# Performance work log

Measured on AMD Instinct MI355X. Metric: run time of the kernel, lower is better.

## Reference

```python
import jax, jax.numpy as jnp
import numpy as np

B, L, H, NT = 16, 2048, 512, 8
HEAD_H = max(32, H // 2)
OUT = 2 * H + NT
LN_EPS = 1e-5


def setup_inputs() -> dict:
    key = jax.random.key(0)
    ks = jax.random.split(key, 32)
    def w(i, shape):
        fan_in = shape[0] if len(shape) > 1 else shape[0]
        return jax.random.normal(ks[i], shape, jnp.float32) / np.sqrt(fan_in)
    z = lambda shape: jnp.zeros(shape, jnp.float32)
    return {
        "x": jax.random.normal(ks[0], (B, L, 2), jnp.float32),
        "t": jax.random.uniform(ks[1], (B, L, 1), jnp.float32),
        "Wt1": w(2, (1, NT)), "bt1": z((NT,)),
        "Wt2": w(3, (NT, NT)), "bt2": z((NT,)),
        "Wpf": w(4, (2 + NT, H)), "bpf": z((H,)),
        "Wpb": w(5, (2 + NT, H)), "bpb": z((H,)),
        "Wzf": w(6, (H, H)), "bzf": z((H,)),
        "Whf": w(7, (H, H)), "bhf": z((H,)),
        "Wzb": w(8, (H, H)), "bzb": z((H,)),
        "Whb": w(9, (H, H)), "bhb": z((H,)),
        "ln_g": jnp.ones((OUT,), jnp.float32), "ln_b": z((OUT,)),
        "time_scale": jnp.array(5.0, jnp.float32),
        "Wg1": w(10, (OUT, HEAD_H)), "bg1": z((HEAD_H,)),
        "Wg2": w(11, (HEAD_H, 1)), "bg2": z((1,)),
    }


def _mingru_states(xc, Wp, bp, Wz, bz, Wh, bh):
    """Run minGRU over xc (B,L,D); return h_prev states: out[:,ti] = h before step ti."""
    inp = xc @ Wp + bp                      # (B,L,H)
    zg = jax.nn.sigmoid(inp @ Wz + bz)
    h_tilde = jnp.tanh(inp @ Wh + bh)
    a = 1.0 - zg                            # decay
    b = zg * h_tilde                        # input injection
    def step(h, ab):
        h = ab[0] * h + ab[1]
        return h, h
    h0 = jnp.zeros((xc.shape[0], Wh.shape[1]), xc.dtype)
    _, hs = jax.lax.scan(step, h0, (jnp.moveaxis(a, 1, 0), jnp.moveaxis(b, 1, 0)))
    hs = jnp.moveaxis(hs, 0, 1)             # (B,L,H), hs[:,ti] = h after step ti
    # Original stores h_prev at each position -> shift right with zero prefix.
    return jnp.concatenate([jnp.zeros_like(hs[:, :1]), hs[:, :-1]], axis=1)


def reference(x, t, Wt1, bt1, Wt2, bt2, Wpf, bpf, Wpb, bpb,
              Wzf, bzf, Whf, bhf, Wzb, bzb, Whb, bhb,
              ln_g, ln_b, time_scale, Wg1, bg1, Wg2, bg2):
    t_enc = jnp.maximum(t @ Wt1 + bt1, 0.0) @ Wt2 + bt2   # (B,L,NT)
    xc = jnp.concatenate([x, t_enc], axis=-1)              # (B,L,2+NT)
    h_fwd = _mingru_states(xc, Wpf, bpf, Wzf, bzf, Whf, bhf)
    # Backward direction: run scan on time-reversed input, then flip back.
    h_bwd = _mingru_states(xc[:, ::-1], Wpb, bpb, Wzb, bzb, Whb, bhb)[:, ::-1]
    h_bi = jnp.concatenate([h_fwd, h_bwd, t_enc], axis=-1)  # (B,L,OUT)
    mu = jnp.mean(h_bi, axis=-1, keepdims=True)
    var = jnp.mean(jnp.square(h_bi - mu), axis=-1, keepdims=True)
    h_bi = (h_bi - mu) * jax.lax.rsqrt(var + LN_EPS) * ln_g + ln_b
    h_bi = jnp.concatenate([h_bi[..., :-NT], h_bi[..., -NT:] * time_scale], axis=-1)
    hid = jax.nn.gelu(h_bi @ Wg1 + bg1, approximate=False)
    return hid @ Wg2 + bg2                                  # (B,L,1)
```

## Files before the change

kernel.cpp:

```cpp
#include <hip/hip_runtime.h>
#include <hip/hip_bf16.h>
#include <math.h>

#define B_    16
#define L_    2048
#define H_    512
#define NT_   8
#define OUT_  1032
#define KPAD_ 1056
#define HEAD_ 256
#define CH_   16
#define CL_   (L_/CH_)

#define ACH_  136
#define ASTR_ (ACH_*8)

typedef short bf16x8 __attribute__((ext_vector_type(8)));
typedef float f32x4  __attribute__((ext_vector_type(4)));

__device__ __forceinline__ float b2f(unsigned short u) {
    union { unsigned int u32; float f; } v; v.u32 = ((unsigned int)u) << 16; return v.f;
}
__device__ __forceinline__ unsigned short f2b(float f) {
    __hip_bfloat16 h = __float2bfloat16(f);
    return *reinterpret_cast<unsigned short*>(&h);
}
__device__ __forceinline__ float sigmoid_f(float x) {
    return 1.f / (1.f + exp2f(-1.44269504f * x));
}
__device__ __forceinline__ float tanh_f(float x) {
    float e = exp2f(2.88539008f * x);
    return 1.f - 2.f / (e + 1.f);
}
__device__ __forceinline__ float gelu_f(float g) {
    float u  = 0.70710678118654752f * g;
    float ax = fabsf(u);
    float t  = 1.f / (1.f + 0.3275911f * ax);
    float poly = ((((1.061405429f*t - 1.453152027f)*t + 1.421413741f)*t
                   - 0.284496736f)*t + 0.254829592f)*t;
    float e  = exp2f(-1.44269504f * ax * ax);
    float er = 1.f - poly * e;
    er = (u < 0.f) ? -er : er;
    return 0.5f * g * (1.f + er);
}

__global__ __launch_bounds__(256) void kT(const float* __restrict__ in,
                                          unsigned short* __restrict__ out,
                                          int R, int C, int RP)
{
    __shared__ float tile[32][33];
    int c0 = blockIdx.x * 32, r0 = blockIdx.y * 32;
    int tx = threadIdx.x & 31, ty = threadIdx.x >> 5;
    #pragma unroll
    for (int j = 0; j < 32; j += 8) {
        int r = r0 + ty + j, c = c0 + tx;
        tile[ty + j][tx] = (r < R && c < C) ? in[(size_t)r*C + c] : 0.f;
    }
    __syncthreads();
    #pragma unroll
    for (int j = 0; j < 32; j += 8) {
        int c = c0 + ty + j, r = r0 + tx;
        if (c < C && r < RP) out[(size_t)c*RP + r] = f2b(tile[tx][ty + j]);
    }
}

__global__ __launch_bounds__(256) void kP(const float* __restrict__ Wg1,
                                          uint4* __restrict__ P)
{
    int idx = blockIdx.x*256 + threadIdx.x;
    if (idx >= 33*1024) return;
    int kb = idx >> 10;
    int rem = idx & 1023;
    int c  = rem >> 2;
    int kg = rem & 3;
    int k0 = kb*32 + kg*8;
    unsigned short o[8];
    #pragma unroll
    for (int j = 0; j < 8; j++) {
        int k = k0 + j;
        o[j] = (k < OUT_) ? f2b(Wg1[(size_t)k*HEAD_ + c]) : (unsigned short)0;
    }
    P[idx] = *(const uint4*)o;
}

__global__ __launch_bounds__(256) void k1_tenc_inp(
    const float* __restrict__ x, const float* __restrict__ t,
    const float* __restrict__ Wt1, const float* __restrict__ bt1,
    const float* __restrict__ Wt2, const float* __restrict__ bt2,
    const float* __restrict__ Wpf, const float* __restrict__ bpf,
    const float* __restrict__ Wpb, const float* __restrict__ bpb,
    float* __restrict__ t_enc,
    unsigned short* __restrict__ inp_f, unsigned short* __restrict__ inp_b)
{
    int wv = threadIdx.x >> 6, lane = threadIdx.x & 63;
    size_t row = (size_t)blockIdx.x*4 + wv;
    float tv = t[row];
    float r1[NT_], te[NT_];
    #pragma unroll
    for (int k = 0; k < NT_; k++) r1[k] = fmaxf(tv*Wt1[k] + bt1[k], 0.f);
    #pragma unroll
    for (int j = 0; j < NT_; j++) {
        float a = bt2[j];
        #pragma unroll
        for (int k = 0; k < NT_; k++) a = fmaf(r1[k], Wt2[k*NT_+j], a);
        te[j] = a;
    }
    if (lane < NT_) t_enc[row*NT_ + lane] = te[lane];
    float x0 = x[row*2+0], x1 = x[row*2+1];
    int c0 = lane*8;
    float af[8], ab[8];
    #pragma unroll
    for (int j = 0; j < 8; j++) {
        int c = c0 + j;
        af[j] = fmaf(x0, Wpf[c], fmaf(x1, Wpf[H_+c], bpf[c]));
        ab[j] = fmaf(x0, Wpb[c], fmaf(x1, Wpb[H_+c], bpb[c]));
    }
    #pragma unroll
    for (int k = 0; k < NT_; k++) {
        #pragma unroll
        for (int j = 0; j < 8; j++) {
            af[j] = fmaf(te[k], Wpf[(2+k)*H_+c0+j], af[j]);
            ab[j] = fmaf(te[k], Wpb[(2+k)*H_+c0+j], ab[j]);
        }
    }
    unsigned short of[8], ob[8];
    #pragma unroll
    for (int j = 0; j < 8; j++) { of[j] = f2b(af[j]); ob[j] = f2b(ab[j]); }
    *(uint4*)&inp_f[row*H_ + c0] = *(const uint4*)of;
    *(uint4*)&inp_b[row*H_ + c0] = *(const uint4*)ob;
}

__global__ __launch_bounds__(256) void k3_mfma(
    const unsigned short* __restrict__ inp,
    const unsigned short* __restrict__ WzT,
    const unsigned short* __restrict__ WhT,
    const float* __restrict__ bz, const float* __restrict__ bh,
    unsigned int* __restrict__ ab_out, int nwg)
{
    __shared__ __align__(16) unsigned short As[128*40];
    __shared__ __align__(16) unsigned short Zs[64*40];
    __shared__ __align__(16) unsigned short Hs[64*40];
    int tid = threadIdx.x;
    int lane = tid & 63, w = tid >> 6;
    int wm = w >> 1, wn = w & 1;

    int bid = blockIdx.x;
    int cpx = nwg >> 3;
    int tile = (bid & 7) * cpx + (bid >> 3);
    int row0 = (tile >> 3) * 128;
    int n0   = (tile & 7) * 64;

    f32x4 accz[4][2], acch[4][2];
    #pragma unroll
    for (int m = 0; m < 4; m++)
        #pragma unroll
        for (int n = 0; n < 2; n++) {
            accz[m][n] = (f32x4){0.f,0.f,0.f,0.f};
            acch[m][n] = (f32x4){0.f,0.f,0.f,0.f};
        }

    int ar = tid >> 1, aseg = tid & 1;
    int bu = tid & 127;
    int br = bu >> 1, bseg = bu & 1;
    const unsigned short* WT = (tid < 128) ? WzT : WhT;
    unsigned short* BS = (tid < 128) ? Zs : Hs;

    int kg = lane >> 4, lr = lane & 15;

    for (int k0 = 0; k0 < H_; k0 += 32) {
        const uint4* ga = (const uint4*)&inp[(size_t)(row0+ar)*H_ + k0 + aseg*16];
        uint4 va0 = ga[0], va1 = ga[1];
        const uint4* gb = (const uint4*)&WT[(size_t)(n0+br)*H_ + k0 + bseg*16];
        uint4 vb0 = gb[0], vb1 = gb[1];
        __syncthreads();
        *(uint4*)&As[ar*40 + aseg*16]     = va0;
        *(uint4*)&As[ar*40 + aseg*16 + 8] = va1;
        *(uint4*)&BS[br*40 + bseg*16]     = vb0;
        *(uint4*)&BS[br*40 + bseg*16 + 8] = vb1;
        __syncthreads();
        bf16x8 af[4], zf[2], hf[2];
        #pragma unroll
        for (int m = 0; m < 4; m++)
            af[m] = *(const bf16x8*)&As[(wm*64 + m*16 + lr)*40 + kg*8];
        #pragma unroll
        for (int n = 0; n < 2; n++) {
            zf[n] = *(const bf16x8*)&Zs[(wn*32 + n*16 + lr)*40 + kg*8];
            hf[n] = *(const bf16x8*)&Hs[(wn*32 + n*16 + lr)*40 + kg*8];
        }
        #pragma unroll
        for (int m = 0; m < 4; m++)
            #pragma unroll
            for (int n = 0; n < 2; n++) {
                accz[m][n] = __builtin_amdgcn_mfma_f32_16x16x32_bf16(af[m], zf[n], accz[m][n], 0, 0, 0);
                acch[m][n] = __builtin_amdgcn_mfma_f32_16x16x32_bf16(af[m], hf[n], acch[m][n], 0, 0, 0);
            }
    }

    #pragma unroll
    for (int m = 0; m < 4; m++)
        #pragma unroll
        for (int n = 0; n < 2; n++) {
            int colg = n0 + wn*32 + n*16 + lr;
            float bzv = bz[colg], bhv = bh[colg];
            #pragma unroll
            for (int r = 0; r < 4; r++) {
                int rowg = row0 + wm*64 + m*16 + kg*4 + r;
                float zg = sigmoid_f(accz[m][n][r] + bzv);
                float a = 1.f - zg;
                float b = zg * tanh_f(acch[m][n][r] + bhv);
                ab_out[(size_t)rowg*H_ + colg] =
                    (unsigned int)f2b(a) | ((unsigned int)f2b(b) << 16);
            }
        }
}

__global__ __launch_bounds__(256) void k4a(
    unsigned int* __restrict__ ABF, unsigned int* __restrict__ ABB,
    float* __restrict__ Scar, float* __restrict__ Pcar, int nb)
{
    int g = blockIdx.x*256 + threadIdx.x;
    int col   = g & (H_-1);
    int chunk = (g >> 9) & (CH_-1);
    int rest  = g >> 13;
    int bb    = rest % nb;
    int dir   = rest / nb;
    unsigned int* AB = dir ? ABB : ABF;
    size_t base = (size_t)bb * L_ * H_ + col;
    float h = 0.f, pp = 1.f;
    if (dir == 0) {
        int lo = chunk * CL_;
        for (int p = 0; p < CL_; p += 8) {
            unsigned int v[8];
            #pragma unroll
            for (int j = 0; j < 8; j++) v[j] = AB[base + (size_t)(lo+p+j)*H_];
            #pragma unroll
            for (int j = 0; j < 8; j++) {
                size_t idx = base + (size_t)(lo+p+j)*H_;
                float av = b2f((unsigned short)(v[j] & 0xffffu));
                float bv = b2f((unsigned short)(v[j] >> 16));
                AB[idx] = (unsigned int)f2b(h) | ((unsigned int)f2b(pp) << 16);
                h = fmaf(av, h, bv);
                pp *= av;
            }
        }
    } else {
        int hi = chunk * CL_ + CL_ - 1;
        for (int p = 0; p < CL_; p += 8) {
            unsigned int v[8];
            #pragma unroll
            for (int j = 0; j < 8; j++) v[j] = AB[base + (size_t)(hi-p-j)*H_];
            #pragma unroll
            for (int j = 0; j < 8; j++) {
                size_t idx = base + (size_t)(hi-p-j)*H_;
                float av = b2f((unsigned short)(v[j] & 0xffffu));
                float bv = b2f((unsigned short)(v[j] >> 16));
                AB[idx] = (unsigned int)f2b(h) | ((unsigned int)f2b(pp) << 16);
                h = fmaf(av, h, bv);
                pp *= av;
            }
        }
    }
    int ci = ((dir*nb + bb)*CH_ + chunk)*H_ + col;
    Scar[ci] = h; Pcar[ci] = pp;
}

__global__ __launch_bounds__(256) void k4b(
    const float* __restrict__ Scar, const float* __restrict__ Pcar,
    float* __restrict__ Hstart, int nb)
{
    int g = blockIdx.x*256 + threadIdx.x;
    int col  = g & (H_-1);
    int rest = g >> 9;
    int bb   = rest % nb;
    int dir  = rest / nb;
    int baseci = (dir*nb + bb)*CH_;
    float h = 0.f;
    if (dir == 0) {
        for (int c = 0; c < CH_; c++) {
            int ci = (baseci + c)*H_ + col;
            Hstart[ci] = h;
            h = Scar[ci] + Pcar[ci]*h;
        }
    } else {
        for (int c = CH_-1; c >= 0; c--) {
            int ci = (baseci + c)*H_ + col;
            Hstart[ci] = h;
            h = Scar[ci] + Pcar[ci]*h;
        }
    }
}

__global__ __launch_bounds__(256) void k5_fused(
    const unsigned int* __restrict__ SPF, const unsigned int* __restrict__ SPB,
    const float* __restrict__ Hstart,
    const float* __restrict__ tenc,
    const float* __restrict__ ln_g, const float* __restrict__ ln_b,
    const float* __restrict__ tsp,
    const uint4* __restrict__ P,
    const float* __restrict__ bg1, const float* __restrict__ Wg2,
    const float* __restrict__ bg2,
    float* __restrict__ out, int nb)
{
    __shared__ __align__(16) unsigned short A[32*ASTR_];
    __shared__ float red[4][32];
    int tid = threadIdx.x, lane = tid & 63, wv = tid >> 6;
    int kg = lane >> 4, lr = lane & 15;
    int row0 = blockIdx.x * 32;
    float ts = tsp[0];

    int bb    = row0 >> 11;
    int chunk = (row0 & (L_-1)) >> 7;
    int cif = ((bb)*CH_ + chunk)*H_;
    int cib = ((nb + bb)*CH_ + chunk)*H_;
    int c0 = lane*8;
    float4 hfa = *(const float4*)&Hstart[cif + c0];
    float4 hfb = *(const float4*)&Hstart[cif + c0 + 4];
    float4 hba = *(const float4*)&Hstart[cib + c0];
    float4 hbb = *(const float4*)&Hstart[cib + c0 + 4];
    float h0f[8] = {hfa.x,hfa.y,hfa.z,hfa.w,hfb.x,hfb.y,hfb.z,hfb.w};
    float h0b[8] = {hba.x,hba.y,hba.z,hba.w,hbb.x,hbb.y,hbb.z,hbb.w};

    float gf[8], bf_[8], gb_[8], bb_[8];
    #pragma unroll
    for (int j = 0; j < 8; j++) {
        gf[j]  = ln_g[c0+j];     bf_[j] = ln_b[c0+j];
        gb_[j] = ln_g[H_+c0+j];  bb_[j] = ln_b[H_+c0+j];
    }
    float gt = 0.f, bt = 0.f;
    if (lane < NT_) { gt = ln_g[2*H_+lane]; bt = ln_b[2*H_+lane]; }

    #pragma unroll
    for (int i = 0; i < 8; i++) {
        int r = wv*8 + i;
        size_t row = (size_t)row0 + r;
        const uint4* pf = (const uint4*)&SPF[row*H_ + c0];
        uint4 f0 = pf[0], f1 = pf[1];
        const uint4* pb = (const uint4*)&SPB[row*H_ + c0];
        uint4 b0 = pb[0], b1 = pb[1];
        unsigned int fwv[8] = {f0.x,f0.y,f0.z,f0.w,f1.x,f1.y,f1.z,f1.w};
        unsigned int bwv[8] = {b0.x,b0.y,b0.z,b0.w,b1.x,b1.y,b1.z,b1.w};
        float fv[8], bv[8];
        float S = 0.f, Q = 0.f;
        #pragma unroll
        for (int j = 0; j < 8; j++) {
            fv[j] = fmaf(b2f((unsigned short)(fwv[j] >> 16)), h0f[j],
                         b2f((unsigned short)(fwv[j] & 0xffffu)));
            S += fv[j]; Q += fv[j]*fv[j];
            bv[j] = fmaf(b2f((unsigned short)(bwv[j] >> 16)), h0b[j],
                         b2f((unsigned short)(bwv[j] & 0xffffu)));
            S += bv[j]; Q += bv[j]*bv[j];
        }
        float tv = 0.f;
        if (lane < NT_) { tv = tenc[row*NT_ + lane]; S += tv; Q += tv*tv; }
        #pragma unroll
        for (int off = 32; off > 0; off >>= 1) {
            S += __shfl_xor(S, off, 64);
            Q += __shfl_xor(Q, off, 64);
        }
        float mu = S * (1.f/1032.f);
        float rs = rsqrtf(Q * (1.f/1032.f) - mu*mu + 1e-5f);
        int key = r & 7;
        unsigned short o[8];
        #pragma unroll
        for (int j = 0; j < 8; j++) o[j] = f2b((fv[j]-mu)*rs*gf[j] + bf_[j]);
        *(uint4*)&A[r*ASTR_ + ((lane ^ key)*8)] = *(const uint4*)o;
        #pragma unroll
        for (int j = 0; j < 8; j++) o[j] = f2b((bv[j]-mu)*rs*gb_[j] + bb_[j]);
        *(uint4*)&A[r*ASTR_ + (((64+lane) ^ key)*8)] = *(const uint4*)o;
        if (lane < NT_) {
            A[r*ASTR_ + ((128 ^ key)*8) + lane] =
                f2b(((tv-mu)*rs*gt + bt) * ts);
        } else if (lane < 32) {
            int byte = 2064 + 2*(lane-8);
            int cc = byte >> 4, rem = (byte & 15) >> 1;
            A[r*ASTR_ + ((cc ^ key)*8) + rem] = 0;
        }
    }
    __syncthreads();

    f32x4 acc[2][4];
    #pragma unroll
    for (int m = 0; m < 2; m++)
        #pragma unroll
        for (int n = 0; n < 4; n++) acc[m][n] = (f32x4){0.f,0.f,0.f,0.f};

    const uint4* Pw = P + wv*256 + lr*4 + kg;
    int keyA = lr & 7;
    for (int kb = 0; kb < 33; kb++) {
        bf16x8 bfv[4];
        #pragma unroll
        for (int n = 0; n < 4; n++)
            bfv[n] = *(const bf16x8*)&Pw[kb*1024 + n*64];
        int ch = kb*4 + kg;
        bf16x8 af0 = *(const bf16x8*)&A[lr*ASTR_      + ((ch ^ keyA)*8)];
        bf16x8 af1 = *(const bf16x8*)&A[(16+lr)*ASTR_ + ((ch ^ keyA)*8)];
        #pragma unroll
        for (int n = 0; n < 4; n++) {
            acc[0][n] = __builtin_amdgcn_mfma_f32_16x16x32_bf16(af0, bfv[n], acc[0][n], 0, 0, 0);
            acc[1][n] = __builtin_amdgcn_mfma_f32_16x16x32_bf16(af1, bfv[n], acc[1][n], 0, 0, 0);
        }
    }

    float rsum[2][4] = {{0.f,0.f,0.f,0.f},{0.f,0.f,0.f,0.f}};
    #pragma unroll
    for (int n = 0; n < 4; n++) {
        int colg = wv*64 + n*16 + lr;
        float bgv = bg1[colg], w2v = Wg2[colg];
        #pragma unroll
        for (int m = 0; m < 2; m++)
            #pragma unroll
            for (int r = 0; r < 4; r++) {
                float gv = gelu_f(acc[m][n][r] + bgv);
                rsum[m][r] = fmaf(gv, w2v, rsum[m][r]);
            }
    }
    #pragma unroll
    for (int off = 1; off < 16; off <<= 1)
        #pragma unroll
        for (int m = 0; m < 2; m++)
            #pragma unroll
            for (int r = 0; r < 4; r++)
                rsum[m][r] += __shfl_xor(rsum[m][r], off, 64);
    if (lr == 0) {
        #pragma unroll
        for (int m = 0; m < 2; m++)
            #pragma unroll
            for (int r = 0; r < 4; r++)
                red[wv][m*16 + kg*4 + r] = rsum[m][r];
    }
    __syncthreads();
    if (tid < 32)
        out[row0 + tid] = red[0][tid] + red[1][tid] + red[2][tid] + red[3][tid] + bg2[0];
}

extern "C" void kernel_launch(void* const* d_in, const int* in_sizes, int n_in,
                              void* d_out, int out_size, void* d_ws, size_t ws_size,
                              hipStream_t stream)
{
    const float* x    = (const float*)d_in[0];
    const float* t    = (const float*)d_in[1];
    const float* Wt1  = (const float*)d_in[2];
    const float* bt1  = (const float*)d_in[3];
    const float* Wt2  = (const float*)d_in[4];
    const float* bt2  = (const float*)d_in[5];
    const float* Wpf  = (const float*)d_in[6];
    const float* bpf  = (const float*)d_in[7];
    const float* Wpb  = (const float*)d_in[8];
    const float* bpb  = (const float*)d_in[9];
    const float* Wzf  = (const float*)d_in[10];
    const float* bzf  = (const float*)d_in[11];
    const float* Whf  = (const float*)d_in[12];
    const float* bhf  = (const float*)d_in[13];
    const float* Wzb  = (const float*)d_in[14];
    const float* bzb  = (const float*)d_in[15];
    const float* Whb  = (const float*)d_in[16];
    const float* bhb  = (const float*)d_in[17];
    const float* ln_g = (const float*)d_in[18];
    const float* ln_b = (const float*)d_in[19];
    const float* tsc  = (const float*)d_in[20];
    const float* Wg1  = (const float*)d_in[21];
    const float* bg1  = (const float*)d_in[22];
    const float* Wg2  = (const float*)d_in[23];
    const float* bg2  = (const float*)d_in[24];
    float* out = (float*)d_out;

    char* p = (char*)d_ws;
    auto carve = [&](size_t bytes) -> char* {
        char* q = p; p += (bytes + 255) & ~(size_t)255; return q;
    };

    unsigned short* WzTf = (unsigned short*)carve((size_t)H_*H_*2);
    unsigned short* WhTf = (unsigned short*)carve((size_t)H_*H_*2);
    unsigned short* WzTb = (unsigned short*)carve((size_t)H_*H_*2);
    unsigned short* WhTb = (unsigned short*)carve((size_t)H_*H_*2);
    uint4*          Pg   = (uint4*)carve((size_t)33*1024*16);

    const size_t perBatch = (size_t)L_*H_*2*2
                          + (size_t)L_*H_*4*2
                          + (size_t)L_*NT_*4
                          + (size_t)CH_*H_*4*3*2;
    size_t fixedUsed = (size_t)(p - (char*)d_ws) + 64*1024;
    int NB = B_;
    while (NB > 1 && fixedUsed + (size_t)NB*perBatch > ws_size) NB >>= 1;

    unsigned short* inpF = (unsigned short*)carve((size_t)NB*L_*H_*2);
    unsigned short* inpB = (unsigned short*)carve((size_t)NB*L_*H_*2);
    unsigned int*   ABF  = (unsigned int*)carve((size_t)NB*L_*H_*4);
    unsigned int*   ABB  = (unsigned int*)carve((size_t)NB*L_*H_*4);
    float* tenc   = (float*)carve((size_t)NB*L_*NT_*4);
    float* Scar   = (float*)carve((size_t)2*NB*CH_*H_*4);
    float* Pcar   = (float*)carve((size_t)2*NB*CH_*H_*4);
    float* Hstart = (float*)carve((size_t)2*NB*CH_*H_*4);

    {
        dim3 g(H_/32, H_/32);
        kT<<<g, 256, 0, stream>>>(Wzf, WzTf, H_, H_, H_);
        kT<<<g, 256, 0, stream>>>(Whf, WhTf, H_, H_, H_);
        kT<<<g, 256, 0, stream>>>(Wzb, WzTb, H_, H_, H_);
        kT<<<g, 256, 0, stream>>>(Whb, WhTb, H_, H_, H_);
        kP<<<132, 256, 0, stream>>>(Wg1, Pg);
    }

    for (int b0 = 0; b0 < B_; b0 += NB) {
        int rows = NB * L_;
        k1_tenc_inp<<<rows/4, 256, 0, stream>>>(
            x + (size_t)b0*L_*2, t + (size_t)b0*L_,
            Wt1, bt1, Wt2, bt2, Wpf, bpf, Wpb, bpb,
            tenc, inpF, inpB);

        int nwg3 = (rows/128) * (H_/64);
        k3_mfma<<<nwg3, 256, 0, stream>>>(inpF, WzTf, WhTf, bzf, bhf, ABF, nwg3);
        k3_mfma<<<nwg3, 256, 0, stream>>>(inpB, WzTb, WhTb, bzb, bhb, ABB, nwg3);

        int scanThreads = 2*NB*H_*CH_;
        k4a<<<scanThreads/256, 256, 0, stream>>>(ABF, ABB, Scar, Pcar, NB);
        k4b<<<(2*NB*H_)/256, 256, 0, stream>>>(Scar, Pcar, Hstart, NB);

        k5_fused<<<rows/32, 256, 0, stream>>>(
            ABF, ABB, Hstart, tenc, ln_g, ln_b, tsc,
            Pg, bg1, Wg2, bg2, out + (size_t)b0*L_, NB);
    }
}
```

Baseline: 314.9 us.

## Shrink k5 row tile to 16, prefetch inputs, and double-buffer weight loads

The fused layernorm+head kernel now handles 16 rows per block instead of 32. This doubles the grid size, and launch bounds are set to allow 4 blocks per CU. All SPF/SPB/tenc loads for a wave's rows are issued up front before the normalization math, to overlap memory latency. The MFMA K-loop software-pipelines the global weight fragment loads with two register buffers. The trade-off is half as much reuse of each Wg1 fragment per block, so global/L2 weight traffic roughly doubles.

After: 374.1 us. 18.8% more time.

```diff
diff --git a/kernel.cpp b/kernel.cpp
--- a/kernel.cpp
+++ b/kernel.cpp
@@ -14,6 +14,7 @@
 
 #define ACH_  136
 #define ASTR_ (ACH_*8)
+#define RB5_  16
 
 typedef short bf16x8 __attribute__((ext_vector_type(8)));
 typedef float f32x4  __attribute__((ext_vector_type(4)));
@@ -250,6 +251,8 @@
             #pragma unroll
             for (int j = 0; j < 8; j++) v[j] = AB[base + (size_t)(hi-p-j)*H_];
             #pragma unroll
+            for (int j = 7; j >= 0; j--) { }
+            #pragma unroll
             for (int j = 0; j < 8; j++) {
                 size_t idx = base + (size_t)(hi-p-j)*H_;
                 float av = b2f((unsigned short)(v[j] & 0xffffu));
@@ -290,7 +293,7 @@
     }
 }
 
-__global__ __launch_bounds__(256) void k5_fused(
+__global__ __launch_bounds__(256, 4) void k5_fused(
     const unsigned int* __restrict__ SPF, const unsigned int* __restrict__ SPB,
     const float* __restrict__ Hstart,
     const float* __restrict__ tenc,
@@ -301,11 +304,11 @@
     const float* __restrict__ bg2,
     float* __restrict__ out, int nb)
 {
-    __shared__ __align__(16) unsigned short A[32*ASTR_];
-    __shared__ float red[4][32];
+    __shared__ __align__(16) unsigned short A[RB5_*ASTR_];
+    __shared__ float red[4][RB5_];
     int tid = threadIdx.x, lane = tid & 63, wv = tid >> 6;
     int kg = lane >> 4, lr = lane & 15;
-    int row0 = blockIdx.x * 32;
+    int row0 = blockIdx.x * RB5_;
     float ts = tsp[0];
 
     int bb    = row0 >> 11;
@@ -320,6 +323,22 @@
     float h0f[8] = {hfa.x,hfa.y,hfa.z,hfa.w,hfb.x,hfb.y,hfb.z,hfb.w};
     float h0b[8] = {hba.x,hba.y,hba.z,hba.w,hbb.x,hbb.y,hbb.z,hbb.w};
 
+    uint4 F0[4], F1[4], G0[4], G1[4];
+    float tvv[4];
+    #pragma unroll
+    for (int i = 0; i < 4; i++) {
+        size_t row = (size_t)row0 + wv*4 + i;
+        const uint4* pf = (const uint4*)&SPF[row*H_ + c0];
+        F0[i] = pf[0]; F1[i] = pf[1];
+        const uint4* pb = (const uint4*)&SPB[row*H_ + c0];
+        G0[i] = pb[0]; G1[i] = pb[1];
+    }
+    #pragma unroll
+    for (int i = 0; i < 4; i++) {
+        size_t row = (size_t)row0 + wv*4 + i;
+        tvv[i] = (lane < NT_) ? tenc[row*NT_ + lane] : 0.f;
+    }
+
     float gf[8], bf_[8], gb_[8], bb_[8];
     #pragma unroll
     for (int j = 0; j < 8; j++) {
@@ -330,15 +349,12 @@
     if (lane < NT_) { gt = ln_g[2*H_+lane]; bt = ln_b[2*H_+lane]; }
 
     #pragma unroll
-    for (int i = 0; i < 8; i++) {
-        int r = wv*8 + i;
-        size_t row = (size_t)row0 + r;
-        const uint4* pf = (const uint4*)&SPF[row*H_ + c0];
-        uint4 f0 = pf[0], f1 = pf[1];
-        const uint4* pb = (const uint4*)&SPB[row*H_ + c0];
-        uint4 b0 = pb[0], b1 = pb[1];
-        unsigned int fwv[8] = {f0.x,f0.y,f0.z,f0.w,f1.x,f1.y,f1.z,f1.w};
-        unsigned int bwv[8] = {b0.x,b0.y,b0.z,b0.w,b1.x,b1.y,b1.z,b1.w};
+    for (int i = 0; i < 4; i++) {
+        int r = wv*4 + i;
+        unsigned int fwv[8] = {F0[i].x,F0[i].y,F0[i].z,F0[i].w,
+                               F1[i].x,F1[i].y,F1[i].z,F1[i].w};
+        unsigned int bwv[8] = {G0[i].x,G0[i].y,G0[i].z,G0[i].w,
+                               G1[i].x,G1[i].y,G1[i].z,G1[i].w};
         float fv[8], bv[8];
         float S = 0.f, Q = 0.f;
         #pragma unroll
@@ -350,8 +366,8 @@
                          b2f((unsigned short)(bwv[j] & 0xffffu)));
             S += bv[j]; Q += bv[j]*bv[j];
         }
-        float tv = 0.f;
-        if (lane < NT_) { tv = tenc[row*NT_ + lane]; S += tv; Q += tv*tv; }
+        float tv = tvv[i];
+        S += tv; Q += tv*tv;
         #pragma unroll
         for (int off = 32; off > 0; off >>= 1) {
             S += __shfl_xor(S, off, 64);
@@ -378,58 +394,70 @@
     }
     __syncthreads();
 
-    f32x4 acc[2][4];
-    #pragma unroll
-    for (int m = 0; m < 2; m++)
-        #pragma unroll
-        for (int n = 0; n < 4; n++) acc[m][n] = (f32x4){0.f,0.f,0.f,0.f};
+    f32x4 acc[4];
+    #pragma unroll
+    for (int n = 0; n < 4; n++) acc[n] = (f32x4){0.f,0.f,0.f,0.f};
 
     const uint4* Pw = P + wv*256 + lr*4 + kg;
     int keyA = lr & 7;
-    for (int kb = 0; kb < 33; kb++) {
-        bf16x8 bfv[4];
-        #pragma unroll
-        for (int n = 0; n < 4; n++)
-            bfv[n] = *(const bf16x8*)&Pw[kb*1024 + n*64];
-        int ch = kb*4 + kg;
-        bf16x8 af0 = *(const bf16x8*)&A[lr*ASTR_      + ((ch ^ keyA)*8)];
-        bf16x8 af1 = *(const bf16x8*)&A[(16+lr)*ASTR_ + ((ch ^ keyA)*8)];
-        #pragma unroll
-        for (int n = 0; n < 4; n++) {
-            acc[0][n] = __builtin_amdgcn_mfma_f32_16x16x32_bf16(af0, bfv[n], acc[0][n], 0, 0, 0);
-            acc[1][n] = __builtin_amdgcn_mfma_f32_16x16x32_bf16(af1, bfv[n], acc[1][n], 0, 0, 0);
-        }
-    }
-
-    float rsum[2][4] = {{0.f,0.f,0.f,0.f},{0.f,0.f,0.f,0.f}};
+    int arow = lr*ASTR_;
+
+#define LOADB(v0,v1,v2,v3,KB) do { \
+        const uint4* q_ = Pw + (KB)*1024; \
+        v0 = *(const bf16x8*)&q_[0]; \
+        v1 = *(const bf16x8*)&q_[64]; \
+        v2 = *(const bf16x8*)&q_[128]; \
+        v3 = *(const bf16x8*)&q_[192]; \
+    } while(0)
+#define LDSA(KB) (*(const bf16x8*)&A[arow + ((((KB)*4+kg) ^ keyA)*8)])
+#define MFMA4(v0,v1,v2,v3,af_) do { \
+        acc[0] = __builtin_amdgcn_mfma_f32_16x16x32_bf16(af_, v0, acc[0],0,0,0); \
+        acc[1] = __builtin_amdgcn_mfma_f32_16x16x32_bf16(af_, v1, acc[1],0,0,0); \
+        acc[2] = __builtin_amdgcn_mfma_f32_16x16x32_bf16(af_, v2, acc[2],0,0,0); \
+        acc[3] = __builtin_amdgcn_mfma_f32_16x16x32_bf16(af_, v3, acc[3],0,0,0); \
+    } while(0)
+
+    bf16x8 a0,a1,a2,a3, d0,d1,d2,d3;
+    LOADB(a0,a1,a2,a3, 0);
+    for (int kb = 0; kb < 32; kb += 2) {
+        LOADB(d0,d1,d2,d3, kb+1);
+        bf16x8 af = LDSA(kb);
+        MFMA4(a0,a1,a2,a3, af);
+        LOADB(a0,a1,a2,a3, kb+2);
+        af = LDSA(kb+1);
+        MFMA4(d0,d1,d2,d3, af);
+    }
+    {
+        bf16x8 af = LDSA(32);
+        MFMA4(a0,a1,a2,a3, af);
+    }
+#undef LOADB
+#undef LDSA
+#undef MFMA4
+
+    float rsum[4] = {0.f,0.f,0.f,0.f};
     #pragma unroll
     for (int n = 0; n < 4; n++) {
         int colg = wv*64 + n*16 + lr;
         float bgv = bg1[colg], w2v = Wg2[colg];
         #pragma unroll
-        for (int m = 0; m < 2; m++)
-            #pragma unroll
-            for (int r = 0; r < 4; r++) {
-                float gv = gelu_f(acc[m][n][r] + bgv);
-                rsum[m][r] = fmaf(gv, w2v, rsum[m][r]);
-            }
+        for (int r = 0; r < 4; r++) {
+            float gv = gelu_f(acc[n][r] + bgv);
+            rsum[r] = fmaf(gv, w2v, rsum[r]);
+        }
     }
     #pragma unroll
     for (int off = 1; off < 16; off <<= 1)
         #pragma unroll
-        for (int m = 0; m < 2; m++)
-            #pragma unroll
-            for (int r = 0; r < 4; r++)
-                rsum[m][r] += __shfl_xor(rsum[m][r], off, 64);
+        for (int r = 0; r < 4; r++)
+            rsum[r] += __shfl_xor(rsum[r], off, 64);
     if (lr == 0) {
         #pragma unroll
-        for (int m = 0; m < 2; m++)
-            #pragma unroll
-            for (int r = 0; r < 4; r++)
-                red[wv][m*16 + kg*4 + r] = rsum[m][r];
+        for (int r = 0; r < 4; r++)
+            red[wv][kg*4 + r] = rsum[r];
     }
     __syncthreads();
-    if (tid < 32)
+    if (tid < RB5_)
         out[row0 + tid] = red[0][tid] + red[1][tid] + red[2][tid] + red[3][tid] + bg2[0];
 }
 
@@ -516,7 +544,7 @@
         k4a<<<scanThreads/256, 256, 0, stream>>>(ABF, ABB, Scar, Pcar, NB);
         k4b<<<(2*NB*H_)/256, 256, 0, stream>>>(Scar, Pcar, Hstart, NB);
 
-        k5_fused<<<rows/32, 256, 0, stream>>>(
+        k5_fused<<<rows/RB5_, 256, 0, stream>>>(
             ABF, ABB, Hstart, tenc, ln_g, ln_b, tsc,
             Pg, bg1, Wg2, bg2, out + (size_t)b0*L_, NB);
     }
```

## Concatenate Wz/Wh into one GEMM, move gate activations into scan kernel, prefetch loads

Applied to the files above, without the earlier changes.

The gate GEMM now multiplies by a concatenated [Wz|Wh] weight with 128x128 tiles and writes raw bf16 pre-activations to a 1024-wide buffer. The sigmoid/tanh and bias application move into the chunked scan kernel, which stores h and the prefix product as separate bf16 halves. The single input buffer is reused by running the projection kernel once per direction. Global loads are register-prefetched in the GEMM, the head GEMM loop is software-pipelined with double-buffered B fragments, and k5 hoists its row loads. This trades extra kernel launches and redundant t_enc work for fewer memory buffers and better MFMA tile reuse.

Measured after the change: 309.0 us. Within noise of the previous version (-1.9%).

```diff
diff --git a/kernel.cpp b/kernel.cpp
--- a/kernel.cpp
+++ b/kernel.cpp
@@ -11,9 +11,11 @@
 #define HEAD_ 256
 #define CH_   16
 #define CL_   (L_/CH_)
+#define NW_   1024
 
 #define ACH_  136
 #define ASTR_ (ACH_*8)
+#define RB5_  32
 
 typedef short bf16x8 __attribute__((ext_vector_type(8)));
 typedef float f32x4  __attribute__((ext_vector_type(4)));
@@ -87,10 +89,9 @@
     const float* __restrict__ x, const float* __restrict__ t,
     const float* __restrict__ Wt1, const float* __restrict__ bt1,
     const float* __restrict__ Wt2, const float* __restrict__ bt2,
-    const float* __restrict__ Wpf, const float* __restrict__ bpf,
-    const float* __restrict__ Wpb, const float* __restrict__ bpb,
+    const float* __restrict__ Wp, const float* __restrict__ bp,
     float* __restrict__ t_enc,
-    unsigned short* __restrict__ inp_f, unsigned short* __restrict__ inp_b)
+    unsigned short* __restrict__ inp)
 {
     int wv = threadIdx.x >> 6, lane = threadIdx.x & 63;
     size_t row = (size_t)blockIdx.x*4 + wv;
@@ -108,114 +109,103 @@
     if (lane < NT_) t_enc[row*NT_ + lane] = te[lane];
     float x0 = x[row*2+0], x1 = x[row*2+1];
     int c0 = lane*8;
-    float af[8], ab[8];
+    float af[8];
     #pragma unroll
     for (int j = 0; j < 8; j++) {
         int c = c0 + j;
-        af[j] = fmaf(x0, Wpf[c], fmaf(x1, Wpf[H_+c], bpf[c]));
-        ab[j] = fmaf(x0, Wpb[c], fmaf(x1, Wpb[H_+c], bpb[c]));
+        af[j] = fmaf(x0, Wp[c], fmaf(x1, Wp[H_+c], bp[c]));
     }
     #pragma unroll
     for (int k = 0; k < NT_; k++) {
         #pragma unroll
-        for (int j = 0; j < 8; j++) {
-            af[j] = fmaf(te[k], Wpf[(2+k)*H_+c0+j], af[j]);
-            ab[j] = fmaf(te[k], Wpb[(2+k)*H_+c0+j], ab[j]);
-        }
-    }
-    unsigned short of[8], ob[8];
-    #pragma unroll
-    for (int j = 0; j < 8; j++) { of[j] = f2b(af[j]); ob[j] = f2b(ab[j]); }
-    *(uint4*)&inp_f[row*H_ + c0] = *(const uint4*)of;
-    *(uint4*)&inp_b[row*H_ + c0] = *(const uint4*)ob;
-}
-
-__global__ __launch_bounds__(256) void k3_mfma(
+        for (int j = 0; j < 8; j++)
+            af[j] = fmaf(te[k], Wp[(2+k)*H_+c0+j], af[j]);
+    }
+    unsigned short of[8];
+    #pragma unroll
+    for (int j = 0; j < 8; j++) of[j] = f2b(af[j]);
+    *(uint4*)&inp[row*H_ + c0] = *(const uint4*)of;
+}
+
+__global__ __launch_bounds__(256) void k3g(
     const unsigned short* __restrict__ inp,
-    const unsigned short* __restrict__ WzT,
-    const unsigned short* __restrict__ WhT,
-    const float* __restrict__ bz, const float* __restrict__ bh,
-    unsigned int* __restrict__ ab_out, int nwg)
+    const unsigned short* __restrict__ WT,
+    unsigned short* __restrict__ zt_out,
+    int nwg)
 {
     __shared__ __align__(16) unsigned short As[128*40];
-    __shared__ __align__(16) unsigned short Zs[64*40];
-    __shared__ __align__(16) unsigned short Hs[64*40];
+    __shared__ __align__(16) unsigned short Bs[128*40];
     int tid = threadIdx.x;
     int lane = tid & 63, w = tid >> 6;
     int wm = w >> 1, wn = w & 1;
+    int kg = lane >> 4, lr = lane & 15;
 
     int bid = blockIdx.x;
     int cpx = nwg >> 3;
     int tile = (bid & 7) * cpx + (bid >> 3);
     int row0 = (tile >> 3) * 128;
-    int n0   = (tile & 7) * 64;
-
-    f32x4 accz[4][2], acch[4][2];
+    int n0   = (tile & 7) * 128;
+
+    f32x4 acc[4][4];
     #pragma unroll
     for (int m = 0; m < 4; m++)
         #pragma unroll
-        for (int n = 0; n < 2; n++) {
-            accz[m][n] = (f32x4){0.f,0.f,0.f,0.f};
-            acch[m][n] = (f32x4){0.f,0.f,0.f,0.f};
-        }
+        for (int n = 0; n < 4; n++) acc[m][n] = (f32x4){0.f,0.f,0.f,0.f};
 
     int ar = tid >> 1, aseg = tid & 1;
-    int bu = tid & 127;
-    int br = bu >> 1, bseg = bu & 1;
-    const unsigned short* WT = (tid < 128) ? WzT : WhT;
-    unsigned short* BS = (tid < 128) ? Zs : Hs;
-
-    int kg = lane >> 4, lr = lane & 15;
+
+    uint4 va0, va1, vb0, vb1;
+    {
+        const uint4* ga = (const uint4*)&inp[(size_t)(row0+ar)*H_ + aseg*16];
+        va0 = ga[0]; va1 = ga[1];
+        const uint4* gb = (const uint4*)&WT[(size_t)(n0+ar)*H_ + aseg*16];
+        vb0 = gb[0]; vb1 = gb[1];
+    }
 
     for (int k0 = 0; k0 < H_; k0 += 32) {
-        const uint4* ga = (const uint4*)&inp[(size_t)(row0+ar)*H_ + k0 + aseg*16];
-        uint4 va0 = ga[0], va1 = ga[1];
-        const uint4* gb = (const uint4*)&WT[(size_t)(n0+br)*H_ + k0 + bseg*16];
-        uint4 vb0 = gb[0], vb1 = gb[1];
         __syncthreads();
         *(uint4*)&As[ar*40 + aseg*16]     = va0;
         *(uint4*)&As[ar*40 + aseg*16 + 8] = va1;
-        *(uint4*)&BS[br*40 + bseg*16]     = vb0;
-        *(uint4*)&BS[br*40 + bseg*16 + 8] = vb1;
+        *(uint4*)&Bs[ar*40 + aseg*16]     = vb0;
+        *(uint4*)&Bs[ar*40 + aseg*16 + 8] = vb1;
         __syncthreads();
-        bf16x8 af[4], zf[2], hf[2];
+        if (k0 + 32 < H_) {
+            const uint4* ga = (const uint4*)&inp[(size_t)(row0+ar)*H_ + k0+32 + aseg*16];
+            va0 = ga[0]; va1 = ga[1];
+            const uint4* gb = (const uint4*)&WT[(size_t)(n0+ar)*H_ + k0+32 + aseg*16];
+            vb0 = gb[0]; vb1 = gb[1];
+        }
+        bf16x8 af[4], bf[4];
         #pragma unroll
         for (int m = 0; m < 4; m++)
             af[m] = *(const bf16x8*)&As[(wm*64 + m*16 + lr)*40 + kg*8];
         #pragma unroll
-        for (int n = 0; n < 2; n++) {
-            zf[n] = *(const bf16x8*)&Zs[(wn*32 + n*16 + lr)*40 + kg*8];
-            hf[n] = *(const bf16x8*)&Hs[(wn*32 + n*16 + lr)*40 + kg*8];
-        }
+        for (int n = 0; n < 4; n++)
+            bf[n] = *(const bf16x8*)&Bs[(wn*64 + n*16 + lr)*40 + kg*8];
         #pragma unroll
         for (int m = 0; m < 4; m++)
             #pragma unroll
-            for (int n = 0; n < 2; n++) {
-                accz[m][n] = __builtin_amdgcn_mfma_f32_16x16x32_bf16(af[m], zf[n], accz[m][n], 0, 0, 0);
-                acch[m][n] = __builtin_amdgcn_mfma_f32_16x16x32_bf16(af[m], hf[n], acch[m][n], 0, 0, 0);
-            }
+            for (int n = 0; n < 4; n++)
+                acc[m][n] = __builtin_amdgcn_mfma_f32_16x16x32_bf16(af[m], bf[n], acc[m][n], 0, 0, 0);
     }
 
     #pragma unroll
     for (int m = 0; m < 4; m++)
         #pragma unroll
-        for (int n = 0; n < 2; n++) {
-            int colg = n0 + wn*32 + n*16 + lr;
-            float bzv = bz[colg], bhv = bh[colg];
+        for (int n = 0; n < 4; n++) {
+            int colg = n0 + wn*64 + n*16 + lr;
             #pragma unroll
             for (int r = 0; r < 4; r++) {
                 int rowg = row0 + wm*64 + m*16 + kg*4 + r;
-                float zg = sigmoid_f(accz[m][n][r] + bzv);
-                float a = 1.f - zg;
-                float b = zg * tanh_f(acch[m][n][r] + bhv);
-                ab_out[(size_t)rowg*H_ + colg] =
-                    (unsigned int)f2b(a) | ((unsigned int)f2b(b) << 16);
+                zt_out[(size_t)rowg*NW_ + colg] = f2b(acc[m][n][r]);
             }
         }
 }
 
 __global__ __launch_bounds__(256) void k4a(
-    unsigned int* __restrict__ ABF, unsigned int* __restrict__ ABB,
+    unsigned short* __restrict__ ATF, unsigned short* __restrict__ ATB,
+    const float* __restrict__ bzf, const float* __restrict__ bhf,
+    const float* __restrict__ bzb, const float* __restrict__ bhb,
     float* __restrict__ Scar, float* __restrict__ Pcar, int nb)
 {
     int g = blockIdx.x*256 + threadIdx.x;
@@ -224,39 +214,51 @@
     int rest  = g >> 13;
     int bb    = rest % nb;
     int dir   = rest / nb;
-    unsigned int* AB = dir ? ABB : ABF;
-    size_t base = (size_t)bb * L_ * H_ + col;
+    unsigned short* AT = dir ? ATB : ATF;
+    float bzv = (dir ? bzb : bzf)[col];
+    float bhv = (dir ? bhb : bhf)[col];
+    size_t base = (size_t)bb * L_ * NW_ + col;
     float h = 0.f, pp = 1.f;
     if (dir == 0) {
         int lo = chunk * CL_;
         for (int p = 0; p < CL_; p += 8) {
-            unsigned int v[8];
-            #pragma unroll
-            for (int j = 0; j < 8; j++) v[j] = AB[base + (size_t)(lo+p+j)*H_];
+            unsigned short zv[8], hv[8];
             #pragma unroll
             for (int j = 0; j < 8; j++) {
-                size_t idx = base + (size_t)(lo+p+j)*H_;
-                float av = b2f((unsigned short)(v[j] & 0xffffu));
-                float bv = b2f((unsigned short)(v[j] >> 16));
-                AB[idx] = (unsigned int)f2b(h) | ((unsigned int)f2b(pp) << 16);
-                h = fmaf(av, h, bv);
-                pp *= av;
+                size_t idx = base + (size_t)(lo+p+j)*NW_;
+                zv[j] = AT[idx]; hv[j] = AT[idx + H_];
+            }
+            #pragma unroll
+            for (int j = 0; j < 8; j++) {
+                size_t idx = base + (size_t)(lo+p+j)*NW_;
+                float zg = sigmoid_f(b2f(zv[j]) + bzv);
+                float a  = 1.f - zg;
+                float bg = zg * tanh_f(b2f(hv[j]) + bhv);
+                AT[idx]      = f2b(h);
+                AT[idx + H_] = f2b(pp);
+                h = fmaf(a, h, bg);
+                pp *= a;
             }
         }
     } else {
         int hi = chunk * CL_ + CL_ - 1;
         for (int p = 0; p < CL_; p += 8) {
-            unsigned int v[8];
-            #pragma unroll
-            for (int j = 0; j < 8; j++) v[j] = AB[base + (size_t)(hi-p-j)*H_];
+            unsigned short zv[8], hv[8];
             #pragma unroll
             for (int j = 0; j < 8; j++) {
-                size_t idx = base + (size_t)(hi-p-j)*H_;
-                float av = b2f((unsigned short)(v[j] & 0xffffu));
-                float bv = b2f((unsigned short)(v[j] >> 16));
-                AB[idx] = (unsigned int)f2b(h) | ((unsigned int)f2b(pp) << 16);
-                h = fmaf(av, h, bv);
-                pp *= av;
+                size_t idx = base + (size_t)(hi-p-j)*NW_;
+                zv[j] = AT[idx]; hv[j] = AT[idx + H_];
+            }
+            #pragma unroll
+            for (int j = 0; j < 8; j++) {
+                size_t idx = base + (size_t)(hi-p-j)*NW_;
+                float zg = sigmoid_f(b2f(zv[j]) + bzv);
+                float a  = 1.f - zg;
+                float bg = zg * tanh_f(b2f(hv[j]) + bhv);
+                AT[idx]      = f2b(h);
+                AT[idx + H_] = f2b(pp);
+                h = fmaf(a, h, bg);
+                pp *= a;
             }
         }
     }
@@ -291,7 +293,7 @@
 }
 
 __global__ __launch_bounds__(256) void k5_fused(
-    const unsigned int* __restrict__ SPF, const unsigned int* __restrict__ SPB,
+    const unsigned short* __restrict__ ATF, const unsigned short* __restrict__ ATB,
     const float* __restrict__ Hstart,
     const float* __restrict__ tenc,
     const float* __restrict__ ln_g, const float* __restrict__ ln_b,
@@ -301,11 +303,11 @@
     const float* __restrict__ bg2,
     float* __restrict__ out, int nb)
 {
-    __shared__ __align__(16) unsigned short A[32*ASTR_];
-    __shared__ float red[4][32];
+    __shared__ __align__(16) unsigned short A[RB5_*ASTR_];
+    __shared__ float red[4][RB5_];
     int tid = threadIdx.x, lane = tid & 63, wv = tid >> 6;
     int kg = lane >> 4, lr = lane & 15;
-    int row0 = blockIdx.x * 32;
+    int row0 = blockIdx.x * RB5_;
     float ts = tsp[0];
 
     int bb    = row0 >> 11;
@@ -320,6 +322,22 @@
     float h0f[8] = {hfa.x,hfa.y,hfa.z,hfa.w,hfb.x,hfb.y,hfb.z,hfb.w};
     float h0b[8] = {hba.x,hba.y,hba.z,hba.w,hbb.x,hbb.y,hbb.z,hbb.w};
 
+    uint4 SF[8], PF[8], SB[8], PB[8];
+    float tvv[8];
+    #pragma unroll
+    for (int i = 0; i < 8; i++) {
+        size_t row = (size_t)row0 + wv*8 + i;
+        SF[i] = *(const uint4*)&ATF[row*NW_ + c0];
+        PF[i] = *(const uint4*)&ATF[row*NW_ + H_ + c0];
+        SB[i] = *(const uint4*)&ATB[row*NW_ + c0];
+        PB[i] = *(const uint4*)&ATB[row*NW_ + H_ + c0];
+    }
+    #pragma unroll
+    for (int i = 0; i < 8; i++) {
+        size_t row = (size_t)row0 + wv*8 + i;
+        tvv[i] = (lane < NT_) ? tenc[row*NT_ + lane] : 0.f;
+    }
+
     float gf[8], bf_[8], gb_[8], bb_[8];
     #pragma unroll
     for (int j = 0; j < 8; j++) {
@@ -332,26 +350,21 @@
     #pragma unroll
     for (int i = 0; i < 8; i++) {
         int r = wv*8 + i;
-        size_t row = (size_t)row0 + r;
-        const uint4* pf = (const uint4*)&SPF[row*H_ + c0];
-        uint4 f0 = pf[0], f1 = pf[1];
-        const uint4* pb = (const uint4*)&SPB[row*H_ + c0];
-        uint4 b0 = pb[0], b1 = pb[1];
-        unsigned int fwv[8] = {f0.x,f0.y,f0.z,f0.w,f1.x,f1.y,f1.z,f1.w};
-        unsigned int bwv[8] = {b0.x,b0.y,b0.z,b0.w,b1.x,b1.y,b1.z,b1.w};
+        const unsigned short* sf = (const unsigned short*)&SF[i];
+        const unsigned short* pf = (const unsigned short*)&PF[i];
+        const unsigned short* sb = (const unsigned short*)&SB[i];
+        const unsigned short* pb = (const unsigned short*)&PB[i];
         float fv[8], bv[8];
         float S = 0.f, Q = 0.f;
         #pragma unroll
         for (int j = 0; j < 8; j++) {
-            fv[j] = fmaf(b2f((unsigned short)(fwv[j] >> 16)), h0f[j],
-                         b2f((unsigned short)(fwv[j] & 0xffffu)));
+            fv[j] = fmaf(b2f(pf[j]), h0f[j], b2f(sf[j]));
             S += fv[j]; Q += fv[j]*fv[j];
-            bv[j] = fmaf(b2f((unsigned short)(bwv[j] >> 16)), h0b[j],
-                         b2f((unsigned short)(bwv[j] & 0xffffu)));
+            bv[j] = fmaf(b2f(pb[j]), h0b[j], b2f(sb[j]));
             S += bv[j]; Q += bv[j]*bv[j];
         }
-        float tv = 0.f;
-        if (lane < NT_) { tv = tenc[row*NT_ + lane]; S += tv; Q += tv*tv; }
+        float tv = tvv[i];
+        S += tv; Q += tv*tv;
         #pragma unroll
         for (int off = 32; off > 0; off >>= 1) {
             S += __shfl_xor(S, off, 64);
@@ -386,20 +399,45 @@
 
     const uint4* Pw = P + wv*256 + lr*4 + kg;
     int keyA = lr & 7;
-    for (int kb = 0; kb < 33; kb++) {
-        bf16x8 bfv[4];
-        #pragma unroll
-        for (int n = 0; n < 4; n++)
-            bfv[n] = *(const bf16x8*)&Pw[kb*1024 + n*64];
-        int ch = kb*4 + kg;
-        bf16x8 af0 = *(const bf16x8*)&A[lr*ASTR_      + ((ch ^ keyA)*8)];
-        bf16x8 af1 = *(const bf16x8*)&A[(16+lr)*ASTR_ + ((ch ^ keyA)*8)];
-        #pragma unroll
-        for (int n = 0; n < 4; n++) {
-            acc[0][n] = __builtin_amdgcn_mfma_f32_16x16x32_bf16(af0, bfv[n], acc[0][n], 0, 0, 0);
-            acc[1][n] = __builtin_amdgcn_mfma_f32_16x16x32_bf16(af1, bfv[n], acc[1][n], 0, 0, 0);
-        }
-    }
+
+#define LOADB(v0,v1,v2,v3,KB) do { \
+        const uint4* q_ = Pw + (KB)*1024; \
+        v0 = *(const bf16x8*)&q_[0]; \
+        v1 = *(const bf16x8*)&q_[64]; \
+        v2 = *(const bf16x8*)&q_[128]; \
+        v3 = *(const bf16x8*)&q_[192]; \
+    } while(0)
+#define LDSA0(KB) (*(const bf16x8*)&A[lr*ASTR_      + ((((KB)*4+kg) ^ keyA)*8)])
+#define LDSA1(KB) (*(const bf16x8*)&A[(16+lr)*ASTR_ + ((((KB)*4+kg) ^ keyA)*8)])
+#define MFMA8(v0,v1,v2,v3,a0_,a1_) do { \
+        acc[0][0] = __builtin_amdgcn_mfma_f32_16x16x32_bf16(a0_, v0, acc[0][0],0,0,0); \
+        acc[0][1] = __builtin_amdgcn_mfma_f32_16x16x32_bf16(a0_, v1, acc[0][1],0,0,0); \
+        acc[0][2] = __builtin_amdgcn_mfma_f32_16x16x32_bf16(a0_, v2, acc[0][2],0,0,0); \
+        acc[0][3] = __builtin_amdgcn_mfma_f32_16x16x32_bf16(a0_, v3, acc[0][3],0,0,0); \
+        acc[1][0] = __builtin_amdgcn_mfma_f32_16x16x32_bf16(a1_, v0, acc[1][0],0,0,0); \
+        acc[1][1] = __builtin_amdgcn_mfma_f32_16x16x32_bf16(a1_, v1, acc[1][1],0,0,0); \
+        acc[1][2] = __builtin_amdgcn_mfma_f32_16x16x32_bf16(a1_, v2, acc[1][2],0,0,0); \
+        acc[1][3] = __builtin_amdgcn_mfma_f32_16x16x32_bf16(a1_, v3, acc[1][3],0,0,0); \
+    } while(0)
+
+    bf16x8 a0,a1,a2,a3, d0,d1,d2,d3;
+    LOADB(a0,a1,a2,a3, 0);
+    for (int kb = 0; kb < 32; kb += 2) {
+        LOADB(d0,d1,d2,d3, kb+1);
+        bf16x8 af0 = LDSA0(kb), af1 = LDSA1(kb);
+        MFMA8(a0,a1,a2,a3, af0, af1);
+        LOADB(a0,a1,a2,a3, kb+2);
+        af0 = LDSA0(kb+1); af1 = LDSA1(kb+1);
+        MFMA8(d0,d1,d2,d3, af0, af1);
+    }
+    {
+        bf16x8 af0 = LDSA0(32), af1 = LDSA1(32);
+        MFMA8(a0,a1,a2,a3, af0, af1);
+    }
+#undef LOADB
+#undef LDSA0
+#undef LDSA1
+#undef MFMA8
 
     float rsum[2][4] = {{0.f,0.f,0.f,0.f},{0.f,0.f,0.f,0.f}};
     #pragma unroll
@@ -429,7 +467,7 @@
                 red[wv][m*16 + kg*4 + r] = rsum[m][r];
     }
     __syncthreads();
-    if (tid < 32)
+    if (tid < RB5_)
         out[row0 + tid] = red[0][tid] + red[1][tid] + red[2][tid] + red[3][tid] + bg2[0];
 }
 
@@ -469,24 +507,21 @@
         char* q = p; p += (bytes + 255) & ~(size_t)255; return q;
     };
 
-    unsigned short* WzTf = (unsigned short*)carve((size_t)H_*H_*2);
-    unsigned short* WhTf = (unsigned short*)carve((size_t)H_*H_*2);
-    unsigned short* WzTb = (unsigned short*)carve((size_t)H_*H_*2);
-    unsigned short* WhTb = (unsigned short*)carve((size_t)H_*H_*2);
-    uint4*          Pg   = (uint4*)carve((size_t)33*1024*16);
-
-    const size_t perBatch = (size_t)L_*H_*2*2
-                          + (size_t)L_*H_*4*2
+    unsigned short* WTf = (unsigned short*)carve((size_t)2*H_*H_*2);
+    unsigned short* WTb = (unsigned short*)carve((size_t)2*H_*H_*2);
+    uint4*          Pg  = (uint4*)carve((size_t)33*1024*16);
+
+    const size_t perBatch = (size_t)L_*H_*2
+                          + (size_t)L_*NW_*2*2
                           + (size_t)L_*NT_*4
                           + (size_t)CH_*H_*4*3*2;
     size_t fixedUsed = (size_t)(p - (char*)d_ws) + 64*1024;
     int NB = B_;
     while (NB > 1 && fixedUsed + (size_t)NB*perBatch > ws_size) NB >>= 1;
 
-    unsigned short* inpF = (unsigned short*)carve((size_t)NB*L_*H_*2);
-    unsigned short* inpB = (unsigned short*)carve((size_t)NB*L_*H_*2);
-    unsigned int*   ABF  = (unsigned int*)carve((size_t)NB*L_*H_*4);
-    unsigned int*   ABB  = (unsigned int*)carve((size_t)NB*L_*H_*4);
+    unsigned short* inp = (unsigned short*)carve((size_t)NB*L_*H_*2);
+    unsigned short* ATF = (unsigned short*)carve((size_t)NB*L_*NW_*2);
+    unsigned short* ATB = (unsigned short*)carve((size_t)NB*L_*NW_*2);
     float* tenc   = (float*)carve((size_t)NB*L_*NT_*4);
     float* Scar   = (float*)carve((size_t)2*NB*CH_*H_*4);
     float* Pcar   = (float*)carve((size_t)2*NB*CH_*H_*4);
@@ -494,30 +529,34 @@
 
     {
         dim3 g(H_/32, H_/32);
-        kT<<<g, 256, 0, stream>>>(Wzf, WzTf, H_, H_, H_);
-        kT<<<g, 256, 0, stream>>>(Whf, WhTf, H_, H_, H_);
-        kT<<<g, 256, 0, stream>>>(Wzb, WzTb, H_, H_, H_);
-        kT<<<g, 256, 0, stream>>>(Whb, WhTb, H_, H_, H_);
+        kT<<<g, 256, 0, stream>>>(Wzf, WTf,            H_, H_, H_);
+        kT<<<g, 256, 0, stream>>>(Whf, WTf + H_*H_,    H_, H_, H_);
+        kT<<<g, 256, 0, stream>>>(Wzb, WTb,            H_, H_, H_);
+        kT<<<g, 256, 0, stream>>>(Whb, WTb + H_*H_,    H_, H_, H_);
         kP<<<132, 256, 0, stream>>>(Wg1, Pg);
     }
 
     for (int b0 = 0; b0 < B_; b0 += NB) {
         int rows = NB * L_;
+        int nwg3 = (rows/128) * 8;
+
         k1_tenc_inp<<<rows/4, 256, 0, stream>>>(
             x + (size_t)b0*L_*2, t + (size_t)b0*L_,
-            Wt1, bt1, Wt2, bt2, Wpf, bpf, Wpb, bpb,
-            tenc, inpF, inpB);
-
-        int nwg3 = (rows/128) * (H_/64);
-        k3_mfma<<<nwg3, 256, 0, stream>>>(inpF, WzTf, WhTf, bzf, bhf, ABF, nwg3);
-        k3_mfma<<<nwg3, 256, 0, stream>>>(inpB, WzTb, WhTb, bzb, bhb, ABB, nwg3);
+            Wt1, bt1, Wt2, bt2, Wpf, bpf, tenc, inp);
+        k3g<<<nwg3, 256, 0, stream>>>(inp, WTf, ATF, nwg3);
+
+        k1_tenc_inp<<<rows/4, 256, 0, stream>>>(
+            x + (size_t)b0*L_*2, t + (size_t)b0*L_,
+            Wt1, bt1, Wt2, bt2, Wpb, bpb, tenc, inp);
+        k3g<<<nwg3, 256, 0, stream>>>(inp, WTb, ATB, nwg3);
 
         int scanThreads = 2*NB*H_*CH_;
-        k4a<<<scanThreads/256, 256, 0, stream>>>(ABF, ABB, Scar, Pcar, NB);
+        k4a<<<scanThreads/256, 256, 0, stream>>>(ATF, ATB, bzf, bhf, bzb, bhb,
+                                                 Scar, Pcar, NB);
         k4b<<<(2*NB*H_)/256, 256, 0, stream>>>(Scar, Pcar, Hstart, NB);
 
-        k5_fused<<<rows/32, 256, 0, stream>>>(
-            ABF, ABB, Hstart, tenc, ln_g, ln_b, tsc,
+        k5_fused<<<rows/RB5_, 256, 0, stream>>>(
+            ATF, ATB, Hstart, tenc, ln_g, ln_b, tsc,
             Pg, bg1, Wg2, bg2, out + (size_t)b0*L_, NB);
     }
 }
```
